# Kernel optimization log

Hardware: AMD Instinct MI355X
Metric: run time of the kernel (lower is better)

The kernel has to match this reference:

```python
import jax, jax.numpy as jnp
import numpy as np

# Dimensions derived from Mamba.__init__: d_model=512 -> joint_latent=32, mamb_latent=D=640
NL, D, DIN, DS, DTR, DC = 4, 640, 1280, 16, 40, 4  # n_layer, d_model, d_inner, d_state, dt_rank, d_conv
B, V = 64, 30  # batch, joint-sequence length (repeat_joint_num)


def _rms(x, w, eps=1e-5):
    return x * jax.lax.rsqrt(jnp.mean(x * x, axis=-1, keepdims=True) + eps) * w


def _mamba_block(x, in_w, conv_w, conv_b, xp_w, dt_w, dt_b, A_log, D_skip, out_w):
    # x: [B, V, D]
    u, res = jnp.split(jnp.einsum('bvd,ed->bve', x, in_w), 2, axis=-1)  # each [B,V,DIN]
    # causal depthwise conv1d over V
    xc = jnp.pad(u.transpose(0, 2, 1), ((0, 0), (0, 0), (DC - 1, 0)))  # [B,DIN,V+DC-1]
    xc = jax.lax.conv_general_dilated(xc, conv_w[:, None, :], (1,), 'VALID',
                                      feature_group_count=DIN,
                                      dimension_numbers=('NCH', 'OIH', 'NCH'))
    u = jax.nn.silu(xc.transpose(0, 2, 1) + conv_b)  # [B,V,DIN]
    # input-dependent SSM params
    dbl = jnp.einsum('bvd,ed->bve', u, xp_w)  # [B,V,DTR+2*DS]
    delta, Bm, Cm = jnp.split(dbl, [DTR, DTR + DS], axis=-1)
    delta = jax.nn.softplus(jnp.einsum('bvr,dr->bvd', delta, dt_w) + dt_b)  # [B,V,DIN]
    A = -jnp.exp(A_log)  # [DIN,DS]
    dA = jnp.exp(delta[..., None] * A)                              # [B,V,DIN,DS]
    dBu = delta[..., None] * Bm[:, :, None, :] * u[..., None]       # [B,V,DIN,DS]

    def step(h, t):
        dA_t, dBu_t, C_t = t
        h = dA_t * h + dBu_t                      # [B,DIN,DS]
        return h, jnp.einsum('bds,bs->bd', h, C_t)

    h0 = jnp.zeros((x.shape[0], DIN, DS), x.dtype)
    _, ys = jax.lax.scan(step, h0, (dA.transpose(1, 0, 2, 3),
                                    dBu.transpose(1, 0, 2, 3),
                                    Cm.transpose(1, 0, 2)))
    y = ys.transpose(1, 0, 2) + u * D_skip        # [B,V,DIN]
    return jnp.einsum('bvd,ed->bve', y * jax.nn.silu(res), out_w)


def setup_inputs() -> dict:
    key = jax.random.key(0)
    ks = jax.random.split(key, 10)
    s = 0.02
    return {
        'x': jax.random.normal(ks[0], (B, V, D), jnp.float32),
        'vs': jax.random.randint(ks[1], (B,), 0, V),
        'norm_w': jnp.ones((NL, D), jnp.float32),
        'in_proj_w': s * jax.random.normal(ks[2], (NL, 2 * DIN, D), jnp.float32),
        'conv_w': s * jax.random.normal(ks[3], (NL, DIN, DC), jnp.float32),
        'conv_b': jnp.zeros((NL, DIN), jnp.float32),
        'x_proj_w': s * jax.random.normal(ks[4], (NL, DTR + 2 * DS, DIN), jnp.float32),
        'dt_proj_w': s * jax.random.normal(ks[5], (NL, DIN, DTR), jnp.float32),
        'dt_proj_b': jnp.full((NL, DIN), -4.0, jnp.float32) + 0.1 * jax.random.normal(ks[6], (NL, DIN), jnp.float32),
        'A_log': jnp.tile(jnp.log(jnp.arange(1.0, DS + 1.0, dtype=jnp.float32)), (NL, DIN, 1)),
        'D_skip': jnp.ones((NL, DIN), jnp.float32),
        'out_proj_w': s * jax.random.normal(ks[7], (NL, D, DIN), jnp.float32),
        'norm_f_w': jnp.ones((D,), jnp.float32),
    }


def reference(x, vs, norm_w, in_proj_w, conv_w, conv_b, x_proj_w, dt_proj_w,
              dt_proj_b, A_log, D_skip, out_proj_w, norm_f_w):
    bidx = jnp.arange(x.shape[0])[:, None]
    # batch-wise circular permutation over V (circular_permute_v)
    fwd_idx = (jnp.arange(V)[None, :] + V - vs[:, None]) % V  # [B,V]
    h = x[bidx, fwd_idx]
    for i in range(NL):
        h = h + _mamba_block(_rms(h, norm_w[i]), in_proj_w[i], conv_w[i], conv_b[i],
                             x_proj_w[i], dt_proj_w[i], dt_proj_b[i], A_log[i],
                             D_skip[i], out_proj_w[i])
    h = _rms(h, norm_f_w)
    # reverse_circular_permute_v
    rev_idx = (jnp.arange(V)[None, :] + vs[:, None]) % V
    return h[bidx, rev_idx]
```

## Files before the change

kernel.cpp:

```cpp
#include <hip/hip_runtime.h>
#include <math.h>

#define NLAYER 4
#define DMODEL 640
#define DINNER 1280
#define DSTATE 16
#define DTRANK 40
#define DCONV  4
#define BATCH  64
#define SEQ    30
#define MTOK   (BATCH*SEQ)
#define NPROJ  (2*DINNER)
#define NDBL   (DTRANK+2*DSTATE)
#define NDBLP  80
#define KSEGS  8
#define KSEG   (DINNER/KSEGS)
#define DTKP   64

#define Q1 (NLAYER*NPROJ*DMODEL/4)
#define Q2 (NLAYER*DMODEL*DINNER/4)
#define Q3 (NLAYER*NDBLP*DINNER/4)
#define Q4 (NLAYER*DINNER*DTKP/4)
#define WCTOT (Q1+Q2+Q3+Q4)

typedef unsigned short u16;
typedef __bf16 bf16x8 __attribute__((ext_vector_type(8)));
typedef float  f32x4  __attribute__((ext_vector_type(4)));
typedef unsigned short u16x8 __attribute__((ext_vector_type(8)));

__device__ __forceinline__ float siluf(float x) {
    return x / (1.0f + __expf(-x));
}

__device__ __forceinline__ u16 f2bf(float f) {
    unsigned int u = __float_as_uint(f);
    u += 0x7fffu + ((u >> 16) & 1u);
    return (u16)(u >> 16);
}

__device__ __forceinline__ float bf2f(u16 b) {
    return __uint_as_float(((unsigned int)b) << 16);
}

__global__ void k_permute(const float* __restrict__ x, const int* __restrict__ vs,
                          float* __restrict__ h) {
    int idx = blockIdx.x * blockDim.x + threadIdx.x;
    if (idx >= MTOK * DMODEL) return;
    int d  = idx % DMODEL;
    int mv = idx / DMODEL;
    int v  = mv % SEQ;
    int b  = mv / SEQ;
    int src = (v + SEQ - vs[b]) % SEQ;
    h[idx] = x[(b * SEQ + src) * DMODEL + d];
}

__global__ __launch_bounds__(256)
void k_wconv(const float* __restrict__ in_w, const float* __restrict__ out_w,
             const float* __restrict__ xp_w, const float* __restrict__ dt_w,
             u16* __restrict__ wbi, u16* __restrict__ wbo,
             u16* __restrict__ wbx, u16* __restrict__ wdt) {
    int i = blockIdx.x * 256 + threadIdx.x;
    if (i < Q1) {
        int j = i * 4;
        float4 v = *(const float4*)(in_w + j);
        ushort4 o;
        o.x = f2bf(v.x); o.y = f2bf(v.y); o.z = f2bf(v.z); o.w = f2bf(v.w);
        *(ushort4*)(wbi + j) = o;
    } else if (i < Q1 + Q2) {
        int j = (i - Q1) * 4;
        float4 v = *(const float4*)(out_w + j);
        ushort4 o;
        o.x = f2bf(v.x); o.y = f2bf(v.y); o.z = f2bf(v.z); o.w = f2bf(v.w);
        *(ushort4*)(wbo + j) = o;
    } else if (i < Q1 + Q2 + Q3) {
        int j = (i - Q1 - Q2) * 4;
        int layer = j / (NDBLP * DINNER);
        int rem   = j % (NDBLP * DINNER);
        int r = rem / DINNER, c = rem % DINNER;
        ushort4 o = make_ushort4(0, 0, 0, 0);
        if (r < NDBL) {
            float4 v = *(const float4*)(xp_w + ((size_t)layer * NDBL + r) * DINNER + c);
            o.x = f2bf(v.x); o.y = f2bf(v.y); o.z = f2bf(v.z); o.w = f2bf(v.w);
        }
        *(ushort4*)(wbx + j) = o;
    } else {
        int j = (i - Q1 - Q2 - Q3) * 4;
        int ld = j / DTKP;
        int c  = j % DTKP;
        ushort4 o = make_ushort4(0, 0, 0, 0);
        if (c < DTRANK) {
            float4 v = *(const float4*)(dt_w + (size_t)ld * DTRANK + c);
            o.x = f2bf(v.x); o.y = f2bf(v.y); o.z = f2bf(v.z); o.w = f2bf(v.w);
        }
        *(ushort4*)(wdt + j) = o;
    }
}

__global__ __launch_bounds__(64)
void k_rmsnorm(const float* __restrict__ h, const float* __restrict__ w,
               u16* __restrict__ xn) {
    int m = blockIdx.x;
    int t = threadIdx.x;
    const float* row = h + (size_t)m * DMODEL;
    float2 vv[5];
    float ss = 0.f;
    #pragma unroll
    for (int i = 0; i < 5; ++i) {
        vv[i] = *(const float2*)(row + i * 128 + t * 2);
        ss += vv[i].x * vv[i].x + vv[i].y * vv[i].y;
    }
    #pragma unroll
    for (int o = 32; o > 0; o >>= 1) ss += __shfl_xor(ss, o, 64);
    float sc = rsqrtf(ss / DMODEL + 1e-5f);
    u16* outp = xn + (size_t)m * DMODEL;
    #pragma unroll
    for (int i = 0; i < 5; ++i) {
        int d = i * 128 + t * 2;
        float2 wv = *(const float2*)(w + d);
        ushort2 o;
        o.x = f2bf(vv[i].x * sc * wv.x);
        o.y = f2bf(vv[i].y * sc * wv.y);
        *(ushort2*)(outp + d) = o;
    }
}

__global__ __launch_bounds__(512)
void k_mfma512(const u16* __restrict__ A, int lda,
               const u16* __restrict__ W,
               u16* __restrict__ Cb, int N, int K) {
    __shared__ u16 As[128 * 32];
    __shared__ u16 Bs[128 * 32];
    const int t = threadIdx.x;
    const int w = t >> 6, l = t & 63;
    const int lane15 = l & 15, quad = l >> 4;
    const int wm = w >> 1, wn = w & 1;
    const int m0 = blockIdx.y * 128, n0 = blockIdx.x * 128;

    f32x4 acc[2][4];
    #pragma unroll
    for (int i = 0; i < 2; ++i)
        #pragma unroll
        for (int j = 0; j < 4; ++j)
            acc[i][j] = (f32x4){0.f, 0.f, 0.f, 0.f};

    for (int k0 = 0; k0 < K; k0 += 32) {
        __syncthreads();
        #pragma unroll
        for (int q = 0; q < 2; ++q) {
            int c = q * 512 + t;
            if (c < 512) {
                const u16* ga = A + (size_t)(m0 + (c >> 2)) * lda + k0 + (c & 3) * 8;
                __builtin_amdgcn_global_load_lds(
                    (const __attribute__((address_space(1))) void*)ga,
                    (__attribute__((address_space(3))) void*)&As[c * 8], 16, 0, 0);
            } else {
                int cb = c - 512;
                const u16* gb = W + (size_t)(n0 + (cb >> 2)) * K + k0 + (cb & 3) * 8;
                __builtin_amdgcn_global_load_lds(
                    (const __attribute__((address_space(1))) void*)gb,
                    (__attribute__((address_space(3))) void*)&Bs[cb * 8], 16, 0, 0);
            }
        }
        __syncthreads();

        bf16x8 af[2], bfrag[4];
        #pragma unroll
        for (int i = 0; i < 2; ++i)
            af[i] = *(const bf16x8*)&As[(wm * 32 + i * 16 + lane15) * 32 + quad * 8];
        #pragma unroll
        for (int j = 0; j < 4; ++j)
            bfrag[j] = *(const bf16x8*)&Bs[(wn * 64 + j * 16 + lane15) * 32 + quad * 8];
        #pragma unroll
        for (int i = 0; i < 2; ++i)
            #pragma unroll
            for (int j = 0; j < 4; ++j)
                acc[i][j] = __builtin_amdgcn_mfma_f32_16x16x32_bf16(
                    af[i], bfrag[j], acc[i][j], 0, 0, 0);
    }

    #pragma unroll
    for (int i = 0; i < 2; ++i) {
        #pragma unroll
        for (int r = 0; r < 4; ++r) {
            int row = m0 + wm * 32 + i * 16 + quad * 4 + r;
            #pragma unroll
            for (int j = 0; j < 4; ++j) {
                int col = n0 + wn * 64 + j * 16 + lane15;
                Cb[(size_t)row * N + col] = f2bf(acc[i][j][r]);
            }
        }
    }
}

__global__ __launch_bounds__(256)
void k_mfma64(const u16* __restrict__ A, int lda,
              const u16* __restrict__ W,
              const float* __restrict__ resid,
              float* __restrict__ C, int N, int K) {
    __shared__ u16 As[64 * 32];
    __shared__ u16 Bs[64 * 32];
    const int t = threadIdx.x;
    const int w = t >> 6, l = t & 63;
    const int lane15 = l & 15, quad = l >> 4;
    const int wm = w >> 1, wn = w & 1;
    const int m0 = blockIdx.y * 64, n0 = blockIdx.x * 64;

    f32x4 acc[2][2];
    #pragma unroll
    for (int i = 0; i < 2; ++i)
        #pragma unroll
        for (int j = 0; j < 2; ++j)
            acc[i][j] = (f32x4){0.f, 0.f, 0.f, 0.f};

    for (int k0 = 0; k0 < K; k0 += 32) {
        __syncthreads();
        {
            int c = t;
            const u16* ga = A + (size_t)(m0 + (c >> 2)) * lda + k0 + (c & 3) * 8;
            __builtin_amdgcn_global_load_lds(
                (const __attribute__((address_space(1))) void*)ga,
                (__attribute__((address_space(3))) void*)&As[c * 8], 16, 0, 0);
            const u16* gb = W + (size_t)(n0 + (c >> 2)) * K + k0 + (c & 3) * 8;
            __builtin_amdgcn_global_load_lds(
                (const __attribute__((address_space(1))) void*)gb,
                (__attribute__((address_space(3))) void*)&Bs[c * 8], 16, 0, 0);
        }
        __syncthreads();

        bf16x8 af[2], bfrag[2];
        #pragma unroll
        for (int i = 0; i < 2; ++i)
            af[i] = *(const bf16x8*)&As[(wm * 32 + i * 16 + lane15) * 32 + quad * 8];
        #pragma unroll
        for (int j = 0; j < 2; ++j)
            bfrag[j] = *(const bf16x8*)&Bs[(wn * 32 + j * 16 + lane15) * 32 + quad * 8];
        #pragma unroll
        for (int i = 0; i < 2; ++i)
            #pragma unroll
            for (int j = 0; j < 2; ++j)
                acc[i][j] = __builtin_amdgcn_mfma_f32_16x16x32_bf16(
                    af[i], bfrag[j], acc[i][j], 0, 0, 0);
    }

    #pragma unroll
    for (int i = 0; i < 2; ++i) {
        #pragma unroll
        for (int r = 0; r < 4; ++r) {
            int row = m0 + wm * 32 + i * 16 + quad * 4 + r;
            #pragma unroll
            for (int j = 0; j < 2; ++j) {
                int col = n0 + wn * 32 + j * 16 + lane15;
                size_t idx = (size_t)row * N + col;
                float v = acc[i][j][r];
                if (resid) v += resid[idx];
                C[idx] = v;
            }
        }
    }
}

__global__ __launch_bounds__(256)
void k_conv(const u16* __restrict__ urb, const float* __restrict__ cw,
            const float* __restrict__ cb, u16* __restrict__ ubf) {
    int idx = blockIdx.x * 256 + threadIdx.x;
    int c = idx % DINNER;
    int b = idx / DINNER;
    const u16* up = urb + (size_t)(b * SEQ) * NPROJ + c;
    float xv[SEQ];
    #pragma unroll
    for (int v = 0; v < SEQ; ++v) xv[v] = bf2f(up[(size_t)v * NPROJ]);
    float w0 = cw[c * 4 + 0], w1 = cw[c * 4 + 1];
    float w2 = cw[c * 4 + 2], w3 = cw[c * 4 + 3];
    float bias = cb[c];
    u16* op = ubf + (size_t)(b * SEQ) * DINNER + c;
    float x0 = 0.f, x1 = 0.f, x2 = 0.f;
    #pragma unroll
    for (int v = 0; v < SEQ; ++v) {
        float x3 = xv[v];
        float o = bias + w0 * x0 + w1 * x1 + w2 * x2 + w3 * x3;
        op[(size_t)v * DINNER] = f2bf(siluf(o));
        x0 = x1; x1 = x2; x2 = x3;
    }
}

__global__ __launch_bounds__(256)
void k_xproj(const u16* __restrict__ ubf, const u16* __restrict__ wbx,
             float* __restrict__ dblp) {
    __shared__ u16 As[64 * 32];
    __shared__ u16 Bs[NDBLP * 32];
    const int t = threadIdx.x;
    const int w = t >> 6, l = t & 63;
    const int lane15 = l & 15, quad = l >> 4;
    const int seg = blockIdx.x;
    const int m0 = blockIdx.y * 64;
    const int kb = seg * KSEG;

    f32x4 acc[5];
    #pragma unroll
    for (int j = 0; j < 5; ++j) acc[j] = (f32x4){0.f, 0.f, 0.f, 0.f};

    for (int k0 = 0; k0 < KSEG; k0 += 32) {
        __syncthreads();
        {
            int c = t;
            const u16* ga = ubf + (size_t)(m0 + (c >> 2)) * DINNER + kb + k0 + (c & 3) * 8;
            __builtin_amdgcn_global_load_lds(
                (const __attribute__((address_space(1))) void*)ga,
                (__attribute__((address_space(3))) void*)&As[c * 8], 16, 0, 0);
            const u16* gb = wbx + (size_t)(c >> 2) * DINNER + kb + k0 + (c & 3) * 8;
            __builtin_amdgcn_global_load_lds(
                (const __attribute__((address_space(1))) void*)gb,
                (__attribute__((address_space(3))) void*)&Bs[c * 8], 16, 0, 0);
        }
        if (t < 64) {
            int c = 256 + t;
            const u16* gb = wbx + (size_t)(c >> 2) * DINNER + kb + k0 + (c & 3) * 8;
            __builtin_amdgcn_global_load_lds(
                (const __attribute__((address_space(1))) void*)gb,
                (__attribute__((address_space(3))) void*)&Bs[c * 8], 16, 0, 0);
        }
        __syncthreads();

        bf16x8 af = *(const bf16x8*)&As[(w * 16 + lane15) * 32 + quad * 8];
        #pragma unroll
        for (int j = 0; j < 5; ++j) {
            bf16x8 bfrag = *(const bf16x8*)&Bs[(j * 16 + lane15) * 32 + quad * 8];
            acc[j] = __builtin_amdgcn_mfma_f32_16x16x32_bf16(af, bfrag, acc[j], 0, 0, 0);
        }
    }

    float* outp = dblp + (size_t)seg * MTOK * NDBLP;
    #pragma unroll
    for (int r = 0; r < 4; ++r) {
        int row = m0 + w * 16 + quad * 4 + r;
        #pragma unroll
        for (int j = 0; j < 5; ++j) {
            int col = j * 16 + lane15;
            outp[(size_t)row * NDBLP + col] = acc[j][r];
        }
    }
}

__global__ __launch_bounds__(256)
void k_dtgemm(const float* __restrict__ dblp, const u16* __restrict__ dtwb,
              const float* __restrict__ dtb, u16* __restrict__ delta) {
    __shared__ u16 As[64 * 32];
    __shared__ u16 Bs[64 * 32];
    const int t = threadIdx.x;
    const int w = t >> 6, l = t & 63;
    const int lane15 = l & 15, quad = l >> 4;
    const int wm = w >> 1, wn = w & 1;
    const int m0 = blockIdx.y * 64, n0 = blockIdx.x * 64;
    const int row = t >> 2, koff = (t & 3) * 8;
    const int m = m0 + row;

    f32x4 acc[2][2];
    #pragma unroll
    for (int i = 0; i < 2; ++i)
        #pragma unroll
        for (int j = 0; j < 2; ++j)
            acc[i][j] = (f32x4){0.f, 0.f, 0.f, 0.f};

    #pragma unroll
    for (int k0 = 0; k0 < DTKP; k0 += 32) {
        float sums[8] = {0.f, 0.f, 0.f, 0.f, 0.f, 0.f, 0.f, 0.f};
        #pragma unroll
        for (int q = 0; q < 2; ++q) {
            int col = k0 + koff + q * 4;
            if (col < DTRANK) {
                #pragma unroll
                for (int sg = 0; sg < KSEGS; ++sg) {
                    float4 p = *(const float4*)&dblp[(size_t)sg * MTOK * NDBLP
                                                     + (size_t)m * NDBLP + col];
                    sums[q * 4 + 0] += p.x; sums[q * 4 + 1] += p.y;
                    sums[q * 4 + 2] += p.z; sums[q * 4 + 3] += p.w;
                }
            }
        }
        u16x8 av;
        #pragma unroll
        for (int e = 0; e < 8; ++e) av[e] = f2bf(sums[e]);
        __syncthreads();
        *(u16x8*)&As[row * 32 + koff] = av;
        {
            int c = t;
            const u16* gb = dtwb + (size_t)(n0 + (c >> 2)) * DTKP + k0 + (c & 3) * 8;
            __builtin_amdgcn_global_load_lds(
                (const __attribute__((address_space(1))) void*)gb,
                (__attribute__((address_space(3))) void*)&Bs[c * 8], 16, 0, 0);
        }
        __syncthreads();

        bf16x8 af[2], bfrag[2];
        #pragma unroll
        for (int i = 0; i < 2; ++i)
            af[i] = *(const bf16x8*)&As[(wm * 32 + i * 16 + lane15) * 32 + quad * 8];
        #pragma unroll
        for (int j = 0; j < 2; ++j)
            bfrag[j] = *(const bf16x8*)&Bs[(wn * 32 + j * 16 + lane15) * 32 + quad * 8];
        #pragma unroll
        for (int i = 0; i < 2; ++i)
            #pragma unroll
            for (int j = 0; j < 2; ++j)
                acc[i][j] = __builtin_amdgcn_mfma_f32_16x16x32_bf16(
                    af[i], bfrag[j], acc[i][j], 0, 0, 0);
    }

    #pragma unroll
    for (int i = 0; i < 2; ++i) {
        #pragma unroll
        for (int r = 0; r < 4; ++r) {
            int orow = m0 + wm * 32 + i * 16 + quad * 4 + r;
            #pragma unroll
            for (int j = 0; j < 2; ++j) {
                int col = n0 + wn * 32 + j * 16 + lane15;
                float vv = acc[i][j][r] + dtb[col];
                vv = (vv > 20.f) ? vv : log1pf(__expf(vv));
                delta[(size_t)orow * DINNER + col] = f2bf(vv);
            }
        }
    }
}

__global__ __launch_bounds__(256)
void k_scan(const u16* __restrict__ ubf, const u16* __restrict__ urb,
            const float* __restrict__ dblp, const u16* __restrict__ delta,
            const float* __restrict__ A_log, const float* __restrict__ Dsk,
            u16* __restrict__ y) {
    __shared__ float BC[SEQ][2 * DSTATE];
    const int b  = blockIdx.x / (DINNER / 256);
    const int dc = blockIdx.x % (DINNER / 256);
    const int d  = dc * 256 + threadIdx.x;

    for (int t = threadIdx.x; t < SEQ * 2 * DSTATE; t += 256) {
        int v = t >> 5, s = t & 31;
        float acc = 0.f;
        #pragma unroll
        for (int sg = 0; sg < KSEGS; ++sg)
            acc += dblp[(size_t)sg * MTOK * NDBLP + (size_t)(b * SEQ + v) * NDBLP + DTRANK + s];
        BC[v][s] = acc;
    }
    __syncthreads();

    float dl[SEQ], uu[SEQ], rr[SEQ];
    #pragma unroll
    for (int v = 0; v < SEQ; ++v)
        dl[v] = bf2f(delta[(size_t)(b * SEQ + v) * DINNER + d]);
    #pragma unroll
    for (int v = 0; v < SEQ; ++v)
        uu[v] = bf2f(ubf[(size_t)(b * SEQ + v) * DINNER + d]);
    #pragma unroll
    for (int v = 0; v < SEQ; ++v)
        rr[v] = bf2f(urb[(size_t)(b * SEQ + v) * NPROJ + DINNER + d]);

    float Ar[DSTATE];
    #pragma unroll
    for (int s = 0; s < DSTATE; ++s) Ar[s] = -__expf(A_log[(size_t)d * DSTATE + s]);
    float dsk = Dsk[d];
    float st[DSTATE];
    #pragma unroll
    for (int s = 0; s < DSTATE; ++s) st[s] = 0.f;

    u16* yp = y + (size_t)(b * SEQ) * DINNER + d;

    #pragma unroll
    for (int v = 0; v < SEQ; ++v) {
        float dlt = dl[v];
        float du  = dlt * uu[v];
        float ya0 = 0.f, ya1 = 0.f, ya2 = 0.f, ya3 = 0.f;
        #pragma unroll
        for (int s = 0; s < DSTATE; s += 4) {
            float dA0 = __expf(dlt * Ar[s + 0]);
            float dA1 = __expf(dlt * Ar[s + 1]);
            float dA2 = __expf(dlt * Ar[s + 2]);
            float dA3 = __expf(dlt * Ar[s + 3]);
            st[s + 0] = dA0 * st[s + 0] + du * BC[v][s + 0];
            st[s + 1] = dA1 * st[s + 1] + du * BC[v][s + 1];
            st[s + 2] = dA2 * st[s + 2] + du * BC[v][s + 2];
            st[s + 3] = dA3 * st[s + 3] + du * BC[v][s + 3];
            ya0 += st[s + 0] * BC[v][DSTATE + s + 0];
            ya1 += st[s + 1] * BC[v][DSTATE + s + 1];
            ya2 += st[s + 2] * BC[v][DSTATE + s + 2];
            ya3 += st[s + 3] * BC[v][DSTATE + s + 3];
        }
        float ya = (ya0 + ya1) + (ya2 + ya3);
        yp[(size_t)v * DINNER] = f2bf((ya + uu[v] * dsk) * siluf(rr[v]));
    }
}

__global__ __launch_bounds__(64)
void k_final(const float* __restrict__ h, const int* __restrict__ vs,
             const float* __restrict__ w, float* __restrict__ out) {
    int mv = blockIdx.x;
    int v = mv % SEQ, b = mv / SEQ;
    int src = (v + vs[b]) % SEQ;
    const float* row = h + (size_t)(b * SEQ + src) * DMODEL;
    int t = threadIdx.x;
    float ss = 0.f;
    for (int d = t; d < DMODEL; d += 64) { float x = row[d]; ss += x * x; }
    #pragma unroll
    for (int o = 32; o > 0; o >>= 1) ss += __shfl_xor(ss, o, 64);
    float sc = rsqrtf(ss / DMODEL + 1e-5f);
    float* op = out + (size_t)mv * DMODEL;
    for (int d = t; d < DMODEL; d += 64) op[d] = row[d] * sc * w[d];
}

extern "C" void kernel_launch(void* const* d_in, const int* in_sizes, int n_in,
                              void* d_out, int out_size, void* d_ws, size_t ws_size,
                              hipStream_t stream) {
    const float* x      = (const float*)d_in[0];
    const int*   vs     = (const int*)d_in[1];
    const float* norm_w = (const float*)d_in[2];
    const float* in_w   = (const float*)d_in[3];
    const float* conv_w = (const float*)d_in[4];
    const float* conv_b = (const float*)d_in[5];
    const float* xp_w   = (const float*)d_in[6];
    const float* dt_w   = (const float*)d_in[7];
    const float* dt_b   = (const float*)d_in[8];
    const float* A_log  = (const float*)d_in[9];
    const float* Dsk    = (const float*)d_in[10];
    const float* out_w  = (const float*)d_in[11];
    const float* nfw    = (const float*)d_in[12];
    float* out = (float*)d_out;

    char* p = (char*)d_ws;
    float* h      = (float*)p; p += (size_t)MTOK * DMODEL * 4;
    u16*   xn     = (u16*)p;   p += (size_t)MTOK * DMODEL * 2;
    u16*   urb    = (u16*)p;   p += (size_t)MTOK * NPROJ * 2;
    u16*   ubf    = (u16*)p;   p += (size_t)MTOK * DINNER * 2;
    float* dblp   = (float*)p; p += (size_t)KSEGS * MTOK * NDBLP * 4;
    u16*   deltab = (u16*)p;   p += (size_t)MTOK * DINNER * 2;
    u16*   y      = (u16*)p;   p += (size_t)MTOK * DINNER * 2;
    u16*   wbi4   = (u16*)p;   p += (size_t)NLAYER * NPROJ * DMODEL * 2;
    u16*   wbo4   = (u16*)p;   p += (size_t)NLAYER * DMODEL * DINNER * 2;
    u16*   wbx4   = (u16*)p;   p += (size_t)NLAYER * NDBLP * DINNER * 2;
    u16*   wdt4   = (u16*)p;   p += (size_t)NLAYER * DINNER * DTKP * 2;

    k_wconv<<<WCTOT / 256, 256, 0, stream>>>(
        in_w, out_w, xp_w, dt_w, wbi4, wbo4, wbx4, wdt4);

    k_permute<<<(MTOK * DMODEL + 255) / 256, 256, 0, stream>>>(x, vs, h);

    for (int l = 0; l < NLAYER; ++l) {
        k_rmsnorm<<<MTOK, 64, 0, stream>>>(h, norm_w + (size_t)l * DMODEL, xn);

        k_mfma512<<<dim3(NPROJ / 128, MTOK / 128), 512, 0, stream>>>(
            xn, DMODEL, wbi4 + (size_t)l * NPROJ * DMODEL, urb, NPROJ, DMODEL);

        k_conv<<<BATCH * DINNER / 256, 256, 0, stream>>>(
            urb, conv_w + (size_t)l * DINNER * DCONV, conv_b + (size_t)l * DINNER, ubf);

        k_xproj<<<dim3(KSEGS, MTOK / 64), 256, 0, stream>>>(
            ubf, wbx4 + (size_t)l * NDBLP * DINNER, dblp);

        k_dtgemm<<<dim3(DINNER / 64, MTOK / 64), 256, 0, stream>>>(
            dblp, wdt4 + (size_t)l * DINNER * DTKP,
            dt_b + (size_t)l * DINNER, deltab);

        k_scan<<<BATCH * (DINNER / 256), 256, 0, stream>>>(
            ubf, urb, dblp, deltab,
            A_log + (size_t)l * DINNER * DSTATE, Dsk + (size_t)l * DINNER, y);

        k_mfma64<<<dim3(DMODEL / 64, MTOK / 64), 256, 0, stream>>>(
            y, DINNER, wbo4 + (size_t)l * DMODEL * DINNER, h, h, DMODEL, DINNER);
    }

    k_final<<<MTOK, 64, 0, stream>>>(h, vs, nfw, out);
}
```

Before: 501.5 us.

## Fuse dt projection GEMM with selective scan into one kernel

Merges the dt-projection GEMM (with bias and softplus) into the scan kernel. Each block reduces the split-K x_proj partials for one batch, runs the small MFMA GEMM into LDS, then scans directly from the fp32 delta held in LDS. This drops one launch per layer and the bf16 delta round-trip through global memory, and it keeps delta in fp32. In exchange each block uses much more LDS (about 70KB), which lowers occupancy, and the GEMM is tiled per batch with only 30 of 32 rows valid.

```diff
diff --git a/kernel.cpp b/kernel.cpp
--- a/kernel.cpp
+++ b/kernel.cpp
@@ -342,126 +342,108 @@
 }
 
 __global__ __launch_bounds__(256)
-void k_dtgemm(const float* __restrict__ dblp, const u16* __restrict__ dtwb,
-              const float* __restrict__ dtb, u16* __restrict__ delta) {
-    __shared__ u16 As[64 * 32];
-    __shared__ u16 Bs[64 * 32];
+void k_dtscan(const u16* __restrict__ ubf, const u16* __restrict__ urb,
+              const float* __restrict__ dblp, const u16* __restrict__ dtwb,
+              const float* __restrict__ dtb,
+              const float* __restrict__ A_log, const float* __restrict__ Dsk,
+              u16* __restrict__ y) {
+    __shared__ float dblS[32][NDBLP];
+    __shared__ u16   As[2 * 32 * 32];
+    __shared__ u16   Bs[256 * DTKP];
+    __shared__ float deltaL[32 * 256];
     const int t = threadIdx.x;
+    const int d0 = blockIdx.x * 256;
+    const int b  = blockIdx.y;
     const int w = t >> 6, l = t & 63;
     const int lane15 = l & 15, quad = l >> 4;
-    const int wm = w >> 1, wn = w & 1;
-    const int m0 = blockIdx.y * 64, n0 = blockIdx.x * 64;
-    const int row = t >> 2, koff = (t & 3) * 8;
-    const int m = m0 + row;
-
-    f32x4 acc[2][2];
+
+    for (int e = t; e < 32 * NDBLP; e += 256) {
+        int v = e / NDBLP, col = e % NDBLP;
+        float s = 0.f;
+        if (v < SEQ && col < NDBL) {
+            #pragma unroll
+            for (int sg = 0; sg < KSEGS; ++sg)
+                s += dblp[(size_t)sg * MTOK * NDBLP + (size_t)(b * SEQ + v) * NDBLP + col];
+        }
+        dblS[v][col] = s;
+    }
+    #pragma unroll
+    for (int it = 0; it < 8; ++it) {
+        int c = it * 256 + t;
+        const u16* gb = dtwb + (size_t)(d0 + (c >> 3)) * DTKP + (c & 7) * 8;
+        __builtin_amdgcn_global_load_lds(
+            (const __attribute__((address_space(1))) void*)gb,
+            (__attribute__((address_space(3))) void*)&Bs[c * 8], 16, 0, 0);
+    }
+    __syncthreads();
+
+    for (int e = t; e < 2048; e += 256) {
+        int r = e >> 6, c = e & 63;
+        float val = (c < DTRANK) ? dblS[r][c] : 0.f;
+        As[(c >> 5) * 1024 + r * 32 + (c & 31)] = f2bf(val);
+    }
+    __syncthreads();
+
+    f32x4 acc[2][4];
     #pragma unroll
     for (int i = 0; i < 2; ++i)
         #pragma unroll
-        for (int j = 0; j < 2; ++j)
+        for (int j = 0; j < 4; ++j)
             acc[i][j] = (f32x4){0.f, 0.f, 0.f, 0.f};
-
-    #pragma unroll
-    for (int k0 = 0; k0 < DTKP; k0 += 32) {
-        float sums[8] = {0.f, 0.f, 0.f, 0.f, 0.f, 0.f, 0.f, 0.f};
-        #pragma unroll
-        for (int q = 0; q < 2; ++q) {
-            int col = k0 + koff + q * 4;
-            if (col < DTRANK) {
-                #pragma unroll
-                for (int sg = 0; sg < KSEGS; ++sg) {
-                    float4 p = *(const float4*)&dblp[(size_t)sg * MTOK * NDBLP
-                                                     + (size_t)m * NDBLP + col];
-                    sums[q * 4 + 0] += p.x; sums[q * 4 + 1] += p.y;
-                    sums[q * 4 + 2] += p.z; sums[q * 4 + 3] += p.w;
-                }
+    #pragma unroll
+    for (int ks = 0; ks < 2; ++ks) {
+        bf16x8 af[2];
+        #pragma unroll
+        for (int mt = 0; mt < 2; ++mt)
+            af[mt] = *(const bf16x8*)&As[ks * 1024 + (mt * 16 + lane15) * 32 + quad * 8];
+        #pragma unroll
+        for (int j = 0; j < 4; ++j) {
+            int n = w * 64 + j * 16 + lane15;
+            bf16x8 bf = *(const bf16x8*)&Bs[n * DTKP + ks * 32 + quad * 8];
+            #pragma unroll
+            for (int mt = 0; mt < 2; ++mt)
+                acc[mt][j] = __builtin_amdgcn_mfma_f32_16x16x32_bf16(
+                    af[mt], bf, acc[mt][j], 0, 0, 0);
+        }
+    }
+    #pragma unroll
+    for (int mt = 0; mt < 2; ++mt) {
+        #pragma unroll
+        for (int j = 0; j < 4; ++j) {
+            int col = w * 64 + j * 16 + lane15;
+            float bias = dtb[d0 + col];
+            #pragma unroll
+            for (int r = 0; r < 4; ++r) {
+                int row = mt * 16 + quad * 4 + r;
+                float vv = acc[mt][j][r] + bias;
+                vv = (vv > 20.f) ? vv : log1pf(__expf(vv));
+                deltaL[row * 256 + col] = vv;
             }
         }
-        u16x8 av;
-        #pragma unroll
-        for (int e = 0; e < 8; ++e) av[e] = f2bf(sums[e]);
-        __syncthreads();
-        *(u16x8*)&As[row * 32 + koff] = av;
-        {
-            int c = t;
-            const u16* gb = dtwb + (size_t)(n0 + (c >> 2)) * DTKP + k0 + (c & 3) * 8;
-            __builtin_amdgcn_global_load_lds(
-                (const __attribute__((address_space(1))) void*)gb,
-                (__attribute__((address_space(3))) void*)&Bs[c * 8], 16, 0, 0);
-        }
-        __syncthreads();
-
-        bf16x8 af[2], bfrag[2];
-        #pragma unroll
-        for (int i = 0; i < 2; ++i)
-            af[i] = *(const bf16x8*)&As[(wm * 32 + i * 16 + lane15) * 32 + quad * 8];
-        #pragma unroll
-        for (int j = 0; j < 2; ++j)
-            bfrag[j] = *(const bf16x8*)&Bs[(wn * 32 + j * 16 + lane15) * 32 + quad * 8];
-        #pragma unroll
-        for (int i = 0; i < 2; ++i)
-            #pragma unroll
-            for (int j = 0; j < 2; ++j)
-                acc[i][j] = __builtin_amdgcn_mfma_f32_16x16x32_bf16(
-                    af[i], bfrag[j], acc[i][j], 0, 0, 0);
-    }
-
-    #pragma unroll
-    for (int i = 0; i < 2; ++i) {
-        #pragma unroll
-        for (int r = 0; r < 4; ++r) {
-            int orow = m0 + wm * 32 + i * 16 + quad * 4 + r;
-            #pragma unroll
-            for (int j = 0; j < 2; ++j) {
-                int col = n0 + wn * 32 + j * 16 + lane15;
-                float vv = acc[i][j][r] + dtb[col];
-                vv = (vv > 20.f) ? vv : log1pf(__expf(vv));
-                delta[(size_t)orow * DINNER + col] = f2bf(vv);
-            }
-        }
-    }
-}
-
-__global__ __launch_bounds__(256)
-void k_scan(const u16* __restrict__ ubf, const u16* __restrict__ urb,
-            const float* __restrict__ dblp, const u16* __restrict__ delta,
-            const float* __restrict__ A_log, const float* __restrict__ Dsk,
-            u16* __restrict__ y) {
-    __shared__ float BC[SEQ][2 * DSTATE];
-    const int b  = blockIdx.x / (DINNER / 256);
-    const int dc = blockIdx.x % (DINNER / 256);
-    const int d  = dc * 256 + threadIdx.x;
-
-    for (int t = threadIdx.x; t < SEQ * 2 * DSTATE; t += 256) {
-        int v = t >> 5, s = t & 31;
-        float acc = 0.f;
-        #pragma unroll
-        for (int sg = 0; sg < KSEGS; ++sg)
-            acc += dblp[(size_t)sg * MTOK * NDBLP + (size_t)(b * SEQ + v) * NDBLP + DTRANK + s];
-        BC[v][s] = acc;
     }
     __syncthreads();
 
+    const int dch = d0 + t;
     float dl[SEQ], uu[SEQ], rr[SEQ];
     #pragma unroll
+    for (int v = 0; v < SEQ; ++v) dl[v] = deltaL[v * 256 + t];
+    #pragma unroll
     for (int v = 0; v < SEQ; ++v)
-        dl[v] = bf2f(delta[(size_t)(b * SEQ + v) * DINNER + d]);
+        uu[v] = bf2f(ubf[(size_t)(b * SEQ + v) * DINNER + dch]);
     #pragma unroll
     for (int v = 0; v < SEQ; ++v)
-        uu[v] = bf2f(ubf[(size_t)(b * SEQ + v) * DINNER + d]);
-    #pragma unroll
-    for (int v = 0; v < SEQ; ++v)
-        rr[v] = bf2f(urb[(size_t)(b * SEQ + v) * NPROJ + DINNER + d]);
+        rr[v] = bf2f(urb[(size_t)(b * SEQ + v) * NPROJ + DINNER + dch]);
 
     float Ar[DSTATE];
     #pragma unroll
-    for (int s = 0; s < DSTATE; ++s) Ar[s] = -__expf(A_log[(size_t)d * DSTATE + s]);
-    float dsk = Dsk[d];
+    for (int s = 0; s < DSTATE; ++s)
+        Ar[s] = -__expf(A_log[(size_t)dch * DSTATE + s]);
+    float dsk = Dsk[dch];
     float st[DSTATE];
     #pragma unroll
     for (int s = 0; s < DSTATE; ++s) st[s] = 0.f;
 
-    u16* yp = y + (size_t)(b * SEQ) * DINNER + d;
+    u16* yp = y + (size_t)(b * SEQ) * DINNER + dch;
 
     #pragma unroll
     for (int v = 0; v < SEQ; ++v) {
@@ -474,14 +456,14 @@
             float dA1 = __expf(dlt * Ar[s + 1]);
             float dA2 = __expf(dlt * Ar[s + 2]);
             float dA3 = __expf(dlt * Ar[s + 3]);
-            st[s + 0] = dA0 * st[s + 0] + du * BC[v][s + 0];
-            st[s + 1] = dA1 * st[s + 1] + du * BC[v][s + 1];
-            st[s + 2] = dA2 * st[s + 2] + du * BC[v][s + 2];
-            st[s + 3] = dA3 * st[s + 3] + du * BC[v][s + 3];
-            ya0 += st[s + 0] * BC[v][DSTATE + s + 0];
-            ya1 += st[s + 1] * BC[v][DSTATE + s + 1];
-            ya2 += st[s + 2] * BC[v][DSTATE + s + 2];
-            ya3 += st[s + 3] * BC[v][DSTATE + s + 3];
+            st[s + 0] = dA0 * st[s + 0] + du * dblS[v][DTRANK + s + 0];
+            st[s + 1] = dA1 * st[s + 1] + du * dblS[v][DTRANK + s + 1];
+            st[s + 2] = dA2 * st[s + 2] + du * dblS[v][DTRANK + s + 2];
+            st[s + 3] = dA3 * st[s + 3] + du * dblS[v][DTRANK + s + 3];
+            ya0 += st[s + 0] * dblS[v][DTRANK + DSTATE + s + 0];
+            ya1 += st[s + 1] * dblS[v][DTRANK + DSTATE + s + 1];
+            ya2 += st[s + 2] * dblS[v][DTRANK + DSTATE + s + 2];
+            ya3 += st[s + 3] * dblS[v][DTRANK + DSTATE + s + 3];
         }
         float ya = (ya0 + ya1) + (ya2 + ya3);
         yp[(size_t)v * DINNER] = f2bf((ya + uu[v] * dsk) * siluf(rr[v]));
@@ -529,7 +511,6 @@
     u16*   urb    = (u16*)p;   p += (size_t)MTOK * NPROJ * 2;
     u16*   ubf    = (u16*)p;   p += (size_t)MTOK * DINNER * 2;
     float* dblp   = (float*)p; p += (size_t)KSEGS * MTOK * NDBLP * 4;
-    u16*   deltab = (u16*)p;   p += (size_t)MTOK * DINNER * 2;
     u16*   y      = (u16*)p;   p += (size_t)MTOK * DINNER * 2;
     u16*   wbi4   = (u16*)p;   p += (size_t)NLAYER * NPROJ * DMODEL * 2;
     u16*   wbo4   = (u16*)p;   p += (size_t)NLAYER * DMODEL * DINNER * 2;
@@ -553,12 +534,9 @@
         k_xproj<<<dim3(KSEGS, MTOK / 64), 256, 0, stream>>>(
             ubf, wbx4 + (size_t)l * NDBLP * DINNER, dblp);
 
-        k_dtgemm<<<dim3(DINNER / 64, MTOK / 64), 256, 0, stream>>>(
-            dblp, wdt4 + (size_t)l * DINNER * DTKP,
-            dt_b + (size_t)l * DINNER, deltab);
-
-        k_scan<<<BATCH * (DINNER / 256), 256, 0, stream>>>(
-            ubf, urb, dblp, deltab,
+        k_dtscan<<<dim3(DINNER / 256, BATCH), 256, 0, stream>>>(
+            ubf, urb, dblp, wdt4 + (size_t)l * DINNER * DTKP,
+            dt_b + (size_t)l * DINNER,
             A_log + (size_t)l * DINNER * DSTATE, Dsk + (size_t)l * DINNER, y);
 
         k_mfma64<<<dim3(DMODEL / 64, MTOK / 64), 256, 0, stream>>>(
```

New measurement: 510.5 us. About the same (+1.8%).
